# Performance work log

Measured on AMD Instinct MI355X. Metric: run time of the kernel, lower is better.

Reference implementation:

```python
import jax, jax.numpy as jnp
import numpy as np

B, S, D = 2, 1024, 4096
H, KVH = 32, 8
HD = D // H          # 128
N_REP = H // KVH     # 4
R = 2                # LoRA rank


def setup_inputs() -> dict:
    key = jax.random.key(0)
    ks = jax.random.split(key, 10)
    sc = 0.02
    x = jax.random.normal(ks[0], (B, S, D), jnp.float32)
    wq = jax.random.normal(ks[1], (D, H * HD), jnp.float32) * sc
    wk = jax.random.normal(ks[2], (D, KVH * HD), jnp.float32) * sc
    wv = jax.random.normal(ks[3], (D, KVH * HD), jnp.float32) * sc
    wo = jax.random.normal(ks[4], (H * HD, D), jnp.float32) * sc
    lora_q_a = jax.random.normal(ks[5], (D, R), jnp.float32) * sc
    lora_q_b = jax.random.normal(ks[6], (R, H * HD), jnp.float32) * sc
    lora_v_a = jax.random.normal(ks[7], (D, R), jnp.float32) * sc
    lora_v_b = jax.random.normal(ks[8], (R, KVH * HD), jnp.float32) * sc
    # RoPE frequencies: freqs_cis[t, i] = exp(1j * t * 10000^(-2i/HD))
    inv_freq = 1.0 / (10000.0 ** (jnp.arange(0, HD, 2, dtype=jnp.float32) / HD))  # [HD/2]
    t = jnp.arange(S, dtype=jnp.float32)
    ang = jnp.outer(t, inv_freq)                      # [S, HD/2]
    freqs_cos = jnp.cos(ang)
    freqs_sin = jnp.sin(ang)
    # causal additive mask [1, 1, S, S]
    mask = jnp.triu(jnp.full((S, S), -1e9, jnp.float32), k=1)[None, None]
    return {"x": x, "wq": wq, "wk": wk, "wv": wv, "wo": wo,
            "lora_q_a": lora_q_a, "lora_q_b": lora_q_b,
            "lora_v_a": lora_v_a, "lora_v_b": lora_v_b,
            "freqs_cos": freqs_cos, "freqs_sin": freqs_sin,
            "mask": mask, "start_pos": 0}


def _rope(t, cos, sin):
    # t: [B, S, h, HD]; pairs (even, odd) are (real, imag) of complex halves
    b, s, h, hd = t.shape
    tr = t.reshape(b, s, h, hd // 2, 2)
    a, bb = tr[..., 0], tr[..., 1]
    c = cos[None, :, None, :]
    sn = sin[None, :, None, :]
    out = jnp.stack([a * c - bb * sn, a * sn + bb * c], axis=-1)
    return out.reshape(b, s, h, hd)


def reference(x, wq, wk, wv, wo, lora_q_a, lora_q_b, lora_v_a, lora_v_b,
              freqs_cos, freqs_sin, mask, start_pos):
    # projections + LoRA (note: original Lora_layer applies NO scaling in forward)
    xq = x @ wq + (x @ lora_q_a) @ lora_q_b            # [B,S,H*HD]
    xk = x @ wk                                         # [B,S,KVH*HD]
    xv = x @ wv + (x @ lora_v_a) @ lora_v_b             # [B,S,KVH*HD]
    xq = xq.reshape(B, S, H, HD)
    xk = xk.reshape(B, S, KVH, HD)
    xv = xv.reshape(B, S, KVH, HD)
    xq = _rope(xq, freqs_cos, freqs_sin)
    xk = _rope(xk, freqs_cos, freqs_sin)
    # repeat_kv (GQA expansion): [B,S,KVH,HD] -> [B,S,H,HD]
    k = jnp.repeat(xk, N_REP, axis=2)
    v = jnp.repeat(xv, N_REP, axis=2)
    # attention
    scores = jnp.einsum('bshd,bthd->bhst', xq, k) / np.sqrt(HD).astype(np.float32)
    scores = scores + mask
    probs = jax.nn.softmax(scores.astype(jnp.float32), axis=-1).astype(xq.dtype)
    out = jnp.einsum('bhst,bthd->bshd', probs, v)       # [B,S,H,HD]
    out = out.reshape(B, S, H * HD) @ wo                # [B,S,D]
    return out
```

## Files before the change

### kernel.cpp

```cpp
#include <hip/hip_runtime.h>
#include <stdint.h>

#define B_ 2
#define S_ 1024
#define D_ 4096
#define H_ 32
#define KVH_ 8
#define HD_ 128

typedef short short8 __attribute__((ext_vector_type(8)));
typedef float floatx4 __attribute__((ext_vector_type(4)));

__device__ __forceinline__ ushort f2bf(float f) {
  union { float f; uint32_t u; } v; v.f = f;
  return (ushort)((v.u + 0x7FFFu + ((v.u >> 16) & 1u)) >> 16);
}
__device__ __forceinline__ float bf2f(ushort u) {
  union { uint32_t x; float f; } v; v.x = ((uint32_t)u) << 16; return v.f;
}

__device__ __forceinline__ void gload16(const void* g, void* l) {
  __builtin_amdgcn_global_load_lds((__attribute__((address_space(1))) void*)g,
                                   (__attribute__((address_space(3))) void*)l,
                                   16, 0, 0);
}

__global__ __launch_bounds__(256) void k_cvtlora(const float* __restrict__ x,
                                                 const float* __restrict__ qa,
                                                 const float* __restrict__ va,
                                                 ushort* __restrict__ xb,
                                                 float* __restrict__ xa) {
  const int row = blockIdx.x, t = threadIdx.x;
  const float* xr = x + (size_t)row * D_;
  ushort* xo = xb + (size_t)row * D_;
  float a0 = 0, a1 = 0, a2 = 0, a3 = 0;
#pragma unroll
  for (int it = 0; it < 4; it++) {
    const int i = it * 1024 + t * 4;
    float4 v = *(const float4*)(xr + i);
    ushort o4[4] = {f2bf(v.x), f2bf(v.y), f2bf(v.z), f2bf(v.w)};
    *(uint2*)(xo + i) = *(uint2*)o4;
    float4 q0 = *(const float4*)(qa + 2 * i);
    float4 q1 = *(const float4*)(qa + 2 * i + 4);
    float4 w0 = *(const float4*)(va + 2 * i);
    float4 w1 = *(const float4*)(va + 2 * i + 4);
    a0 += v.x * q0.x + v.y * q0.z + v.z * q1.x + v.w * q1.z;
    a1 += v.x * q0.y + v.y * q0.w + v.z * q1.y + v.w * q1.w;
    a2 += v.x * w0.x + v.y * w0.z + v.z * w1.x + v.w * w1.z;
    a3 += v.x * w0.y + v.y * w0.w + v.z * w1.y + v.w * w1.w;
  }
#pragma unroll
  for (int off = 32; off; off >>= 1) {
    a0 += __shfl_down(a0, off, 64);
    a1 += __shfl_down(a1, off, 64);
    a2 += __shfl_down(a2, off, 64);
    a3 += __shfl_down(a3, off, 64);
  }
  __shared__ float red[4][4];
  const int w = t >> 6, lane = t & 63;
  if (lane == 0) { red[w][0] = a0; red[w][1] = a1; red[w][2] = a2; red[w][3] = a3; }
  __syncthreads();
  if (t < 4)
    xa[(size_t)row * 4 + t] = red[0][t] + red[1][t] + red[2][t] + red[3][t];
}

__global__ __launch_bounds__(256) void k_trw2(const float* __restrict__ in0,
                                              const float* __restrict__ in1,
                                              ushort* __restrict__ out0,
                                              ushort* __restrict__ out1,
                                              int in_stride, int out_stride) {
  const float* in = blockIdx.z ? in1 : in0;
  ushort* out = blockIdx.z ? out1 : out0;
  __shared__ float t[64][65];
  const int n0 = blockIdx.x * 64, k0 = blockIdx.y * 64;
  const int c4 = (threadIdx.x & 15) * 4, r = threadIdx.x >> 4;
#pragma unroll
  for (int rr = 0; rr < 64; rr += 16) {
    float4 v = *(const float4*)&in[(size_t)(k0 + r + rr) * in_stride + n0 + c4];
    t[r + rr][c4] = v.x; t[r + rr][c4 + 1] = v.y;
    t[r + rr][c4 + 2] = v.z; t[r + rr][c4 + 3] = v.w;
  }
  __syncthreads();
#pragma unroll
  for (int rr = 0; rr < 64; rr += 16) {
    const int n = r + rr;
    ushort o4[4] = {f2bf(t[c4][n]), f2bf(t[c4 + 1][n]),
                    f2bf(t[c4 + 2][n]), f2bf(t[c4 + 3][n])};
    *(uint2*)&out[(size_t)(n0 + n) * out_stride + k0 + c4] = *(uint2*)o4;
  }
}

#define GBAR __builtin_amdgcn_s_barrier()
#define VMCNT0 asm volatile("s_waitcnt vmcnt(0)" ::: "memory")
#define VMCNT4 asm volatile("s_waitcnt vmcnt(4)" ::: "memory")
#define VMCNT6 asm volatile("s_waitcnt vmcnt(6)" ::: "memory")

#define QSTG(T, SB) do {                                                     \
    const ushort* ga_ = A + (size_t)(m0 + srow) * Kz + (T) * 32 + ssl;       \
    gload16(ga_, qlds + (SB) * 32768 + w * 1024);                            \
    _Pragma("unroll") for (int u_ = 0; u_ < 3; u_++) {                       \
      const ushort* gb_ = Bt + (size_t)(n0 + u_ * 128 + srow) * Kz + (T) * 32 + ssl; \
      gload16(gb_, qlds + (SB) * 32768 + 8192 + u_ * 8192 + w * 1024);       \
    }                                                                        \
  } while (0)

#define QTILE(T, RB) do {                                                    \
    if ((T) + 2 < 128) QSTG((T) + 2, ((RB) + 2) % 3);                        \
    const char* ab_ = qlds + (RB) * 32768 + (wr * 64 + lr) * 64 + rswz;      \
    _Pragma("unroll") for (int fr = 0; fr < 4; fr++)                         \
      af[fr] = *(const short8*)(ab_ + fr * 1024);                            \
    const char* bb_ = qlds + (RB) * 32768 + 8192 + (wc * 32 + lr) * 64 + rswz; \
    _Pragma("unroll") for (int u_ = 0; u_ < 3; u_++)                         \
    _Pragma("unroll") for (int e_ = 0; e_ < 2; e_++)                         \
      bfr[u_ * 2 + e_] = *(const short8*)(bb_ + u_ * 8192 + e_ * 1024);      \
    __builtin_amdgcn_s_setprio(1);                                           \
    _Pragma("unroll") for (int fr = 0; fr < 4; fr++)                         \
    _Pragma("unroll") for (int u_ = 0; u_ < 6; u_++)                         \
      acc[fr][u_] = __builtin_amdgcn_mfma_f32_16x16x32_bf16(                 \
          af[fr], bfr[u_], acc[fr][u_], 0, 0, 0);                            \
    __builtin_amdgcn_s_setprio(0);                                           \
    if ((T) + 2 < 128) { VMCNT4; } else { VMCNT0; }                          \
    GBAR;                                                                    \
  } while (0)

__global__ __launch_bounds__(512, 2) void k_gemmq(const ushort* __restrict__ A,
                                                  const ushort* __restrict__ Bt,
                                                  ushort* __restrict__ Qb,
                                                  ushort* __restrict__ Kb,
                                                  ushort* __restrict__ Vt,
                                                  const float* __restrict__ xa,
                                                  const float* __restrict__ qb,
                                                  const float* __restrict__ vb,
                                                  const float* __restrict__ fcos,
                                                  const float* __restrict__ fsin) {
  __shared__ char qlds[98304];
  const int flat = blockIdx.y * 16 + blockIdx.x;
  const int swz_id = (flat & 7) * 32 + (flat >> 3);
  const int m0 = (swz_id >> 4) * 128, n0 = (swz_id & 15) * 384;
  const int tid = threadIdx.x, lane = tid & 63, w = tid >> 6;
  const int wr = w >> 2, wc = w & 3;
  const int lr = lane & 15, g = lane >> 4;
  const size_t Kz = 4096;
  const int srow = tid >> 2;
  const int ssl = ((tid & 3) ^ ((srow >> 1) & 3)) * 8;
  const int rswz = (g ^ ((lr >> 1) & 3)) << 4;

  floatx4 acc[4][6] = {};
  short8 af[4], bfr[6];

  QSTG(0, 0); QSTG(1, 1);
  VMCNT4;
  GBAR;

  for (int tt = 0; tt < 126; tt += 3) {
    QTILE(tt + 0, 0);
    QTILE(tt + 1, 1);
    QTILE(tt + 2, 2);
  }
  QTILE(126, 0);
  QTILE(127, 1);

#pragma unroll
  for (int fr = 0; fr < 4; fr++) {
    const int mb = m0 + wr * 64 + fr * 16 + g * 4;
    const int bb = mb >> 10, s0 = mb & 1023;
    float4 xa4[4];
#pragma unroll
    for (int r = 0; r < 4; r++) xa4[r] = *(const float4*)&xa[(size_t)(mb + r) * 4];
#pragma unroll
    for (int j = 0; j < 3; j++)
#pragma unroll
      for (int e = 0; e < 2; e++) {
        const int n = n0 + j * 128 + wc * 32 + e * 16 + lr;
        if (n < 5120) {
          const bool lq = (n < 4096);
          float b0 = 0.f, b1 = 0.f;
          if (lq) { b0 = qb[n]; b1 = qb[4096 + n]; }
          const int p = (n & 127) >> 1;
          const bool even = !(n & 1);
          const int d = n & 127;
          ushort* dst = lq ? (Qb + ((size_t)(bb * H_ + (n >> 7)) * S_) * HD_ + d)
                           : (Kb + ((size_t)(bb * KVH_ + ((n - 4096) >> 7)) * S_) * HD_ + d);
#pragma unroll
          for (int r = 0; r < 4; r++) {
            float cc = acc[fr][j * 2 + e][r];
            if (lq) cc += xa4[r].x * b0 + xa4[r].y * b1;
            float pv = __shfl_xor(cc, 1, 64);
            const int s = s0 + r;
            float c = fcos[s * 64 + p], sn = fsin[s * 64 + p];
            float o = even ? (cc * c - pv * sn) : (cc * c + pv * sn);
            dst[(size_t)s * HD_] = f2bf(o);
          }
        } else {
          const int vcol = n - 5120;
          const float b0 = vb[vcol], b1 = vb[1024 + vcol];
          ushort v4[4];
#pragma unroll
          for (int r = 0; r < 4; r++)
            v4[r] = f2bf(acc[fr][j * 2 + e][r] + xa4[r].z * b0 + xa4[r].w * b1);
          *(uint2*)&Vt[(size_t)((bb * 8 + (vcol >> 7)) * 128 + (vcol & 127)) * 1024 + s0] =
              *(uint2*)v4;
        }
      }
  }
}

#define OSTG(T, SB) do {                                                     \
    const ushort* ga_ = A + (size_t)(m0 + w * 16 + osr) * Kz + (T) * 64 + osc; \
    char* la_ = olds + (SB) * 49152 + w * 2048;                              \
    gload16(ga_, la_); gload16(ga_ + 8 * Kz, la_ + 1024);                    \
    _Pragma("unroll") for (int u_ = 0; u_ < 2; u_++) {                       \
      const ushort* gb_ = Bt + (size_t)(n0 + u_ * 128 + w * 16 + osr) * Kz + (T) * 64 + osc; \
      char* lb_ = olds + (SB) * 49152 + 16384 + u_ * 16384 + w * 2048;       \
      gload16(gb_, lb_); gload16(gb_ + 8 * Kz, lb_ + 1024);                  \
    }                                                                        \
  } while (0)

#define OTILE(T, RB) do {                                                    \
    if ((T) + 2 < 64) OSTG((T) + 2, ((RB) + 2) % 3);                         \
    const char* ab_ = olds + (RB) * 49152 + (wr * 64 + lr) * 128;            \
    _Pragma("unroll") for (int fr = 0; fr < 4; fr++)                         \
    _Pragma("unroll") for (int ks = 0; ks < 2; ks++)                         \
      af[fr][ks] = *(const short8*)(ab_ + fr * 2048 + (((ks * 4 + g) * 16) ^ swz)); \
    const char* bb_ = olds + (RB) * 49152 + 16384 + (wc * 32 + lr) * 128;    \
    _Pragma("unroll") for (int u_ = 0; u_ < 2; u_++)                         \
    _Pragma("unroll") for (int e_ = 0; e_ < 2; e_++)                         \
    _Pragma("unroll") for (int ks = 0; ks < 2; ks++)                         \
      bfr[u_ * 2 + e_][ks] = *(const short8*)(bb_ + u_ * 16384 + e_ * 2048 + (((ks * 4 + g) * 16) ^ swz)); \
    __builtin_amdgcn_s_setprio(1);                                           \
    _Pragma("unroll") for (int fr = 0; fr < 4; fr++)                         \
    _Pragma("unroll") for (int u_ = 0; u_ < 4; u_++)                         \
    _Pragma("unroll") for (int ks = 0; ks < 2; ks++)                         \
      acc[fr][u_] = __builtin_amdgcn_mfma_f32_16x16x32_bf16(                 \
          af[fr][ks], bfr[u_][ks], acc[fr][u_], 0, 0, 0);                    \
    __builtin_amdgcn_s_setprio(0);                                           \
    if ((T) + 2 < 64) { VMCNT6; } else { VMCNT0; }                           \
    GBAR;                                                                    \
  } while (0)

__global__ __launch_bounds__(512, 2) void k_gemmo(const ushort* __restrict__ A,
                                                  const ushort* __restrict__ Bt,
                                                  float* __restrict__ C) {
  __shared__ char olds[147456];
  const int flat = blockIdx.y * 16 + blockIdx.x;
  const int swz_id = (flat & 7) * 32 + (flat >> 3);
  const int m0 = (swz_id >> 4) * 128, n0 = (swz_id & 15) * 256;
  const int tid = threadIdx.x, lane = tid & 63, w = tid >> 6;
  const int wr = w >> 2, wc = w & 3;
  const int lr = lane & 15, g = lane >> 4;
  const int swz = (lr & 7) * 16;
  const size_t Kz = 4096;
  const int osr = lane >> 3;
  const int osc = ((lane & 7) ^ (osr & 7)) * 8;

  floatx4 acc[4][4] = {};
  short8 af[4][2], bfr[4][2];

  OSTG(0, 0); OSTG(1, 1);
  VMCNT6;
  GBAR;

  for (int tt = 0; tt < 63; tt += 3) {
    OTILE(tt + 0, 0);
    OTILE(tt + 1, 1);
    OTILE(tt + 2, 2);
  }
  OTILE(63, 0);

#pragma unroll
  for (int fr = 0; fr < 4; fr++) {
    const int mb = m0 + wr * 64 + fr * 16 + g * 4;
#pragma unroll
    for (int j = 0; j < 2; j++)
#pragma unroll
      for (int e = 0; e < 2; e++) {
        const int n = n0 + j * 128 + wc * 32 + e * 16 + lr;
#pragma unroll
        for (int r = 0; r < 4; r++)
          C[(size_t)(mb + r) * 4096 + n] = acc[fr][j * 2 + e][r];
      }
  }
}

#define FSTAGE(T, DB) do {                                                   \
    _Pragma("unroll") for (int i_ = 0; i_ < 4; i_++) {                       \
      gload16(Kg + (size_t)((T) * 64 + i_ * 16 + k_srow) * HD_ + k_scol,     \
              fls + (DB) * 16384 + i_ * 4096 + w * 1024);                    \
      gload16(Vg + (size_t)(i_ * 32 + v_srow) * S_ + (T) * 64 + v_scol,      \
              fls + 32768 + (DB) * 16384 + i_ * 4096 + w * 1024);            \
    }                                                                        \
  } while (0)

__global__ __launch_bounds__(256, 2) void k_flash(const ushort* __restrict__ Qb,
                                                  const ushort* __restrict__ Kb,
                                                  const ushort* __restrict__ Vt,
                                                  ushort* __restrict__ attn) {
  __shared__ char fls[81920];
  const int qblk = (gridDim.x - 1) - blockIdx.x;
  const int h = blockIdx.y, b = blockIdx.z;
  const int kvh = h >> 2;
  const int tid = threadIdx.x, w = tid >> 6, lane = tid & 63;
  const int lr = lane & 15, g = lane >> 4;
  const int swz = (lr & 7) * 16;
  const int qra = qblk * 128 + w * 16;
  const ushort* Qrow = Qb + ((size_t)(b * H_ + h) * S_ + qra + lr) * HD_;
  short8 qfa[4], qfb[4];
#pragma unroll
  for (int ks = 0; ks < 4; ks++) {
    qfa[ks] = *(const short8*)(Qrow + ks * 32 + g * 8);
    qfb[ks] = *(const short8*)(Qrow + 64 * HD_ + ks * 32 + g * 8);
  }
  const ushort* Kg = Kb + (size_t)(b * KVH_ + kvh) * S_ * HD_;
  const ushort* Vg = Vt + (size_t)(b * KVH_ + kvh) * HD_ * S_;
  char* Pw = fls + 65536 + w * 4096;
  const int q7 = lr & 7;
  const int k_srow = tid >> 4;
  const int k_scol = ((tid & 15) ^ (k_srow & 7)) * 8;
  const int v_srow = tid >> 3;
  const int v_scol = ((tid & 7) ^ (v_srow & 7)) * 8;
  const float scale = 0.088388347648318447f;

  float m_a = -1e30f, l_a = 0.f, m_b = -1e30f, l_b = 0.f;
  floatx4 oa[8] = {}, ob[8] = {};
  const int nt = 2 * qblk + 2;
  const int lastA = 2 * qblk;

  FSTAGE(0, 0);
  VMCNT0;
  GBAR;

  for (int t = 0; t < nt; t++) {
    const int cur = t & 1;
    if (t + 1 < nt) FSTAGE(t + 1, cur ^ 1);
    const char* Kl = fls + cur * 16384;
    const char* Vl = fls + 32768 + cur * 16384;
    if (t <= lastA) {
      floatx4 s4[4] = {};
      __builtin_amdgcn_s_setprio(1);
#pragma unroll
      for (int mf = 0; mf < 4; mf++) {
        const char* Krow = Kl + (mf * 16 + lr) * 256;
#pragma unroll
        for (int ks = 0; ks < 4; ks++) {
          short8 kf = *(const short8*)(Krow + (((ks * 4 + g) * 16) ^ swz));
          s4[mf] = __builtin_amdgcn_mfma_f32_16x16x32_bf16(kf, qfa[ks], s4[mf], 0, 0, 0);
        }
      }
      __builtin_amdgcn_s_setprio(0);
      float tm = -1e30f;
      if (t == lastA) {
#pragma unroll
        for (int mf = 0; mf < 4; mf++)
#pragma unroll
          for (int r = 0; r < 4; r++) {
            int kv = t * 64 + mf * 16 + g * 4 + r;
            float v = (kv > qra + lr) ? -1e30f : s4[mf][r] * scale;
            s4[mf][r] = v; tm = fmaxf(tm, v);
          }
      } else {
#pragma unroll
        for (int mf = 0; mf < 4; mf++)
#pragma unroll
          for (int r = 0; r < 4; r++) {
            float v = s4[mf][r] * scale;
            s4[mf][r] = v; tm = fmaxf(tm, v);
          }
      }
      tm = fmaxf(tm, __shfl_xor(tm, 16, 64));
      tm = fmaxf(tm, __shfl_xor(tm, 32, 64));
      float m_new = fmaxf(m_a, tm);
      float corr = __expf(m_a - m_new);
      float rs = 0.f;
#pragma unroll
      for (int mf = 0; mf < 4; mf++)
#pragma unroll
        for (int r = 0; r < 4; r++) {
          float p = __expf(s4[mf][r] - m_new);
          s4[mf][r] = p; rs += p;
        }
      rs += __shfl_xor(rs, 16, 64);
      rs += __shfl_xor(rs, 32, 64);
      l_a = l_a * corr + rs; m_a = m_new;
#pragma unroll
      for (int r = 0; r < 4; r++) {
        float cr = __shfl(corr, g * 4 + r, 64);
#pragma unroll
        for (int nf = 0; nf < 8; nf++) oa[nf][r] *= cr;
      }
#pragma unroll
      for (int mf = 0; mf < 4; mf++) {
        uint2 pv;
        pv.x = (uint32_t)f2bf(s4[mf][0]) | ((uint32_t)f2bf(s4[mf][1]) << 16);
        pv.y = (uint32_t)f2bf(s4[mf][2]) | ((uint32_t)f2bf(s4[mf][3]) << 16);
        *(uint2*)(Pw + lr * 128 + ((mf * 32 + g * 8) ^ (q7 << 4))) = pv;
      }
    }
    {
      floatx4 s4[4] = {};
      __builtin_amdgcn_s_setprio(1);
#pragma unroll
      for (int mf = 0; mf < 4; mf++) {
        const char* Krow = Kl + (mf * 16 + lr) * 256;
#pragma unroll
        for (int ks = 0; ks < 4; ks++) {
          short8 kf = *(const short8*)(Krow + (((ks * 4 + g) * 16) ^ swz));
          s4[mf] = __builtin_amdgcn_mfma_f32_16x16x32_bf16(kf, qfb[ks], s4[mf], 0, 0, 0);
        }
      }
      __builtin_amdgcn_s_setprio(0);
      float tm = -1e30f;
      if (t == nt - 1) {
#pragma unroll
        for (int mf = 0; mf < 4; mf++)
#pragma unroll
          for (int r = 0; r < 4; r++) {
            int kv = t * 64 + mf * 16 + g * 4 + r;
            float v = (kv > qra + 64 + lr) ? -1e30f : s4[mf][r] * scale;
            s4[mf][r] = v; tm = fmaxf(tm, v);
          }
      } else {
#pragma unroll
        for (int mf = 0; mf < 4; mf++)
#pragma unroll
          for (int r = 0; r < 4; r++) {
            float v = s4[mf][r] * scale;
            s4[mf][r] = v; tm = fmaxf(tm, v);
          }
      }
      tm = fmaxf(tm, __shfl_xor(tm, 16, 64));
      tm = fmaxf(tm, __shfl_xor(tm, 32, 64));
      float m_new = fmaxf(m_b, tm);
      float corr = __expf(m_b - m_new);
      float rs = 0.f;
#pragma unroll
      for (int mf = 0; mf < 4; mf++)
#pragma unroll
        for (int r = 0; r < 4; r++) {
          float p = __expf(s4[mf][r] - m_new);
          s4[mf][r] = p; rs += p;
        }
      rs += __shfl_xor(rs, 16, 64);
      rs += __shfl_xor(rs, 32, 64);
      l_b = l_b * corr + rs; m_b = m_new;
#pragma unroll
      for (int r = 0; r < 4; r++) {
        float cr = __shfl(corr, g * 4 + r, 64);
#pragma unroll
        for (int nf = 0; nf < 8; nf++) ob[nf][r] *= cr;
      }
#pragma unroll
      for (int mf = 0; mf < 4; mf++) {
        uint2 pv;
        pv.x = (uint32_t)f2bf(s4[mf][0]) | ((uint32_t)f2bf(s4[mf][1]) << 16);
        pv.y = (uint32_t)f2bf(s4[mf][2]) | ((uint32_t)f2bf(s4[mf][3]) << 16);
        *(uint2*)(Pw + 2048 + lr * 128 + ((mf * 32 + g * 8) ^ (q7 << 4))) = pv;
      }
    }
    __builtin_amdgcn_s_setprio(1);
#pragma unroll
    for (int ks2 = 0; ks2 < 2; ks2++) {
      short8 pb = *(const short8*)(Pw + 2048 + lr * 128 + ((ks2 * 64 + g * 16) ^ (q7 << 4)));
      short8 pa = pb;
      if (t <= lastA)
        pa = *(const short8*)(Pw + lr * 128 + ((ks2 * 64 + g * 16) ^ (q7 << 4)));
#pragma unroll
      for (int nf = 0; nf < 8; nf++) {
        short8 vf = *(const short8*)(Vl + (nf * 16 + lr) * 128 + (((ks2 * 4 + g) * 16) ^ swz));
        if (t <= lastA)
          oa[nf] = __builtin_amdgcn_mfma_f32_16x16x32_bf16(pa, vf, oa[nf], 0, 0, 0);
        ob[nf] = __builtin_amdgcn_mfma_f32_16x16x32_bf16(pb, vf, ob[nf], 0, 0, 0);
      }
    }
    __builtin_amdgcn_s_setprio(0);
    VMCNT0;
    GBAR;
  }
  const float linva = 1.0f / l_a, linvb = 1.0f / l_b;
  ushort* outp = attn + ((size_t)(b * S_) + qra) * 4096 + h * 128;
#pragma unroll
  for (int r = 0; r < 4; r++) {
    float lia = __shfl(linva, g * 4 + r, 64);
    float lib = __shfl(linvb, g * 4 + r, 64);
    ushort* orow = outp + (size_t)(g * 4 + r) * 4096;
#pragma unroll
    for (int nf = 0; nf < 8; nf++) {
      orow[nf * 16 + lr] = f2bf(oa[nf][r] * lia);
      orow[(size_t)64 * 4096 + nf * 16 + lr] = f2bf(ob[nf][r] * lib);
    }
  }
}

extern "C" void kernel_launch(void* const* d_in, const int* in_sizes, int n_in,
                              void* d_out, int out_size, void* d_ws, size_t ws_size,
                              hipStream_t stream) {
  (void)in_sizes; (void)n_in; (void)out_size; (void)ws_size;
  const float* x    = (const float*)d_in[0];
  const float* wq   = (const float*)d_in[1];
  const float* wk   = (const float*)d_in[2];
  const float* wv   = (const float*)d_in[3];
  const float* wo   = (const float*)d_in[4];
  const float* lqa  = (const float*)d_in[5];
  const float* lqb  = (const float*)d_in[6];
  const float* lva  = (const float*)d_in[7];
  const float* lvb  = (const float*)d_in[8];
  const float* fcos = (const float*)d_in[9];
  const float* fsin = (const float*)d_in[10];

  char* ws = (char*)d_ws;
  ushort* xb   = (ushort*)(ws + 0);
  ushort* wT   = (ushort*)(ws + 16777216);
  ushort* woT  = (ushort*)(ws + 67108864);
  ushort* Qb   = (ushort*)(ws + 150994944);
  ushort* Kb   = (ushort*)(ws + 167772160);
  ushort* Vt   = (ushort*)(ws + 171966464);
  ushort* attn = (ushort*)(ws + 176160768);
  float*  xa   = (float*) (ws + 192937984);

  k_cvtlora<<<2048, 256, 0, stream>>>(x, lqa, lva, xb, xa);
  k_trw2<<<dim3(64, 64, 2), 256, 0, stream>>>(wq, wo, wT, woT, 4096, 4096);
  k_trw2<<<dim3(16, 64, 2), 256, 0, stream>>>(wk, wv, wT + (size_t)4096 * 4096,
                                              wT + (size_t)5120 * 4096, 1024, 4096);
  k_gemmq<<<dim3(16, 16), 512, 0, stream>>>(xb, wT, Qb, Kb, Vt, xa, lqb, lvb,
                                            fcos, fsin);
  k_flash<<<dim3(8, 32, 2), 256, 0, stream>>>(Qb, Kb, Vt, attn);
  k_gemmo<<<dim3(16, 16), 512, 0, stream>>>(attn, woT, (float*)d_out);
}
```

Baseline: 293.9 us.

## Use K=64 double-buffered QKV GEMM tiles and lazy softmax rescaling

The fused QKV projection GEMM now stages K=64 slices per iteration into a two-buffer 128KB LDS ring instead of K=32 slices in a three-buffer ring. This halves the number of barriers and loop iterations, and it uses a new XOR swizzle. The trade-off is a full vmcnt(0) wait each step, which shortens the prefetch distance. Separately, the flash-attention softmax skips the running-max update and the accumulator rescale unless the new tile max exceeds the old one by more than 8 (a threshold in scaled-logit units), saving exp and shuffle work per tile.

```diff
diff --git a/kernel.cpp b/kernel.cpp
--- a/kernel.cpp
+++ b/kernel.cpp
@@ -92,35 +92,18 @@
 
 #define GBAR __builtin_amdgcn_s_barrier()
 #define VMCNT0 asm volatile("s_waitcnt vmcnt(0)" ::: "memory")
-#define VMCNT4 asm volatile("s_waitcnt vmcnt(4)" ::: "memory")
 #define VMCNT6 asm volatile("s_waitcnt vmcnt(6)" ::: "memory")
 
 #define QSTG(T, SB) do {                                                     \
-    const ushort* ga_ = A + (size_t)(m0 + srow) * Kz + (T) * 32 + ssl;       \
-    gload16(ga_, qlds + (SB) * 32768 + w * 1024);                            \
+    const ushort* ga_ = A + (size_t)(m0 + w * 16 + qsr) * Kz + (T) * 64 + qsc; \
+    char* la_ = qlds + (SB) * 65536 + w * 2048;                              \
+    gload16(ga_, la_); gload16(ga_ + 8 * Kz, la_ + 1024);                    \
     _Pragma("unroll") for (int u_ = 0; u_ < 3; u_++) {                       \
-      const ushort* gb_ = Bt + (size_t)(n0 + u_ * 128 + srow) * Kz + (T) * 32 + ssl; \
-      gload16(gb_, qlds + (SB) * 32768 + 8192 + u_ * 8192 + w * 1024);       \
+      const ushort* gb_ = Bt + (size_t)(n0 + u_ * 128 + w * 16 + qsr) * Kz   \
+                          + (T) * 64 + qsc;                                  \
+      char* lb_ = qlds + (SB) * 65536 + 16384 + u_ * 16384 + w * 2048;       \
+      gload16(gb_, lb_); gload16(gb_ + 8 * Kz, lb_ + 1024);                  \
     }                                                                        \
-  } while (0)
-
-#define QTILE(T, RB) do {                                                    \
-    if ((T) + 2 < 128) QSTG((T) + 2, ((RB) + 2) % 3);                        \
-    const char* ab_ = qlds + (RB) * 32768 + (wr * 64 + lr) * 64 + rswz;      \
-    _Pragma("unroll") for (int fr = 0; fr < 4; fr++)                         \
-      af[fr] = *(const short8*)(ab_ + fr * 1024);                            \
-    const char* bb_ = qlds + (RB) * 32768 + 8192 + (wc * 32 + lr) * 64 + rswz; \
-    _Pragma("unroll") for (int u_ = 0; u_ < 3; u_++)                         \
-    _Pragma("unroll") for (int e_ = 0; e_ < 2; e_++)                         \
-      bfr[u_ * 2 + e_] = *(const short8*)(bb_ + u_ * 8192 + e_ * 1024);      \
-    __builtin_amdgcn_s_setprio(1);                                           \
-    _Pragma("unroll") for (int fr = 0; fr < 4; fr++)                         \
-    _Pragma("unroll") for (int u_ = 0; u_ < 6; u_++)                         \
-      acc[fr][u_] = __builtin_amdgcn_mfma_f32_16x16x32_bf16(                 \
-          af[fr], bfr[u_], acc[fr][u_], 0, 0, 0);                            \
-    __builtin_amdgcn_s_setprio(0);                                           \
-    if ((T) + 2 < 128) { VMCNT4; } else { VMCNT0; }                          \
-    GBAR;                                                                    \
   } while (0)
 
 __global__ __launch_bounds__(512, 2) void k_gemmq(const ushort* __restrict__ A,
@@ -133,32 +116,56 @@
                                                   const float* __restrict__ vb,
                                                   const float* __restrict__ fcos,
                                                   const float* __restrict__ fsin) {
-  __shared__ char qlds[98304];
+  __shared__ char qlds[131072];
   const int flat = blockIdx.y * 16 + blockIdx.x;
   const int swz_id = (flat & 7) * 32 + (flat >> 3);
   const int m0 = (swz_id >> 4) * 128, n0 = (swz_id & 15) * 384;
   const int tid = threadIdx.x, lane = tid & 63, w = tid >> 6;
   const int wr = w >> 2, wc = w & 3;
   const int lr = lane & 15, g = lane >> 4;
+  const int swz = (lr & 7) * 16;
   const size_t Kz = 4096;
-  const int srow = tid >> 2;
-  const int ssl = ((tid & 3) ^ ((srow >> 1) & 3)) * 8;
-  const int rswz = (g ^ ((lr >> 1) & 3)) << 4;
+  const int qsr = lane >> 3;
+  const int qsc = ((lane & 7) ^ (qsr & 7)) * 8;
 
   floatx4 acc[4][6] = {};
-  short8 af[4], bfr[6];
-
-  QSTG(0, 0); QSTG(1, 1);
-  VMCNT4;
+  short8 af[4][2], bfr[6][2];
+
+  QSTG(0, 0);
+  VMCNT0;
   GBAR;
 
-  for (int tt = 0; tt < 126; tt += 3) {
-    QTILE(tt + 0, 0);
-    QTILE(tt + 1, 1);
-    QTILE(tt + 2, 2);
-  }
-  QTILE(126, 0);
-  QTILE(127, 1);
+  for (int t = 0; t < 64; ++t) {
+    const int bu = t & 1;
+    if (t + 1 < 64) QSTG(t + 1, bu ^ 1);
+    const char* ab_ = qlds + bu * 65536 + (wr * 64 + lr) * 128;
+#pragma unroll
+    for (int fr = 0; fr < 4; fr++)
+#pragma unroll
+      for (int ks = 0; ks < 2; ks++)
+        af[fr][ks] = *(const short8*)(ab_ + fr * 2048 + (((ks * 4 + g) * 16) ^ swz));
+    const char* bb_ = qlds + bu * 65536 + 16384 + (wc * 32 + lr) * 128;
+#pragma unroll
+    for (int u = 0; u < 3; u++)
+#pragma unroll
+      for (int e = 0; e < 2; e++)
+#pragma unroll
+        for (int ks = 0; ks < 2; ks++)
+          bfr[u * 2 + e][ks] = *(const short8*)(bb_ + u * 16384 + e * 2048 +
+                                                (((ks * 4 + g) * 16) ^ swz));
+    __builtin_amdgcn_s_setprio(1);
+#pragma unroll
+    for (int fr = 0; fr < 4; fr++)
+#pragma unroll
+      for (int u = 0; u < 6; u++)
+#pragma unroll
+        for (int ks = 0; ks < 2; ks++)
+          acc[fr][u] = __builtin_amdgcn_mfma_f32_16x16x32_bf16(
+              af[fr][ks], bfr[u][ks], acc[fr][u], 0, 0, 0);
+    __builtin_amdgcn_s_setprio(0);
+    VMCNT0;
+    GBAR;
+  }
 
 #pragma unroll
   for (int fr = 0; fr < 4; fr++) {
@@ -368,25 +375,29 @@
       }
       tm = fmaxf(tm, __shfl_xor(tm, 16, 64));
       tm = fmaxf(tm, __shfl_xor(tm, 32, 64));
-      float m_new = fmaxf(m_a, tm);
-      float corr = __expf(m_a - m_new);
+      if (!__all(tm - m_a <= 8.f)) {
+        float m_new = fmaxf(m_a, tm);
+        float corr = __expf(m_a - m_new);
+        l_a *= corr;
+#pragma unroll
+        for (int r = 0; r < 4; r++) {
+          float cr = __shfl(corr, g * 4 + r, 64);
+#pragma unroll
+          for (int nf = 0; nf < 8; nf++) oa[nf][r] *= cr;
+        }
+        m_a = m_new;
+      }
       float rs = 0.f;
 #pragma unroll
       for (int mf = 0; mf < 4; mf++)
 #pragma unroll
         for (int r = 0; r < 4; r++) {
-          float p = __expf(s4[mf][r] - m_new);
+          float p = __expf(s4[mf][r] - m_a);
           s4[mf][r] = p; rs += p;
         }
       rs += __shfl_xor(rs, 16, 64);
       rs += __shfl_xor(rs, 32, 64);
-      l_a = l_a * corr + rs; m_a = m_new;
-#pragma unroll
-      for (int r = 0; r < 4; r++) {
-        float cr = __shfl(corr, g * 4 + r, 64);
-#pragma unroll
-        for (int nf = 0; nf < 8; nf++) oa[nf][r] *= cr;
-      }
+      l_a += rs;
 #pragma unroll
       for (int mf = 0; mf < 4; mf++) {
         uint2 pv;
@@ -429,25 +440,29 @@
       }
       tm = fmaxf(tm, __shfl_xor(tm, 16, 64));
       tm = fmaxf(tm, __shfl_xor(tm, 32, 64));
-      float m_new = fmaxf(m_b, tm);
-      float corr = __expf(m_b - m_new);
+      if (!__all(tm - m_b <= 8.f)) {
+        float m_new = fmaxf(m_b, tm);
+        float corr = __expf(m_b - m_new);
+        l_b *= corr;
+#pragma unroll
+        for (int r = 0; r < 4; r++) {
+          float cr = __shfl(corr, g * 4 + r, 64);
+#pragma unroll
+          for (int nf = 0; nf < 8; nf++) ob[nf][r] *= cr;
+        }
+        m_b = m_new;
+      }
       float rs = 0.f;
 #pragma unroll
       for (int mf = 0; mf < 4; mf++)
 #pragma unroll
         for (int r = 0; r < 4; r++) {
-          float p = __expf(s4[mf][r] - m_new);
+          float p = __expf(s4[mf][r] - m_b);
           s4[mf][r] = p; rs += p;
         }
       rs += __shfl_xor(rs, 16, 64);
       rs += __shfl_xor(rs, 32, 64);
-      l_b = l_b * corr + rs; m_b = m_new;
-#pragma unroll
-      for (int r = 0; r < 4; r++) {
-        float cr = __shfl(corr, g * 4 + r, 64);
-#pragma unroll
-        for (int nf = 0; nf < 8; nf++) ob[nf][r] *= cr;
-      }
+      l_b += rs;
 #pragma unroll
       for (int mf = 0; mf < 4; mf++) {
         uint2 pv;
```

After: 1.129 ms. +284.3%, slower.
